# Optimization experiments

Hardware: AMD Instinct MI355X
Metric: run time of the kernel (lower is better)

## Reference

```python
import jax, jax.numpy as jnp
import numpy as np

PAD_ID = 0
B, S, T = 32, 128, 16   # batch, words per sentence, chars per word
VOCAB, E, H = 262, 64, 256


def _lstm_scan(x, w_ih, w_hh, b):
    # x: [T, N, D] -> outputs h: [T, N, H]. PyTorch gate order i, f, g, o.
    N = x.shape[1]
    Hh = w_hh.shape[1]
    init = (jnp.zeros((N, Hh), x.dtype), jnp.zeros((N, Hh), x.dtype))

    def step(carry, xt):
        h, c = carry
        g = xt @ w_ih.T + h @ w_hh.T + b
        i, f, gg, o = jnp.split(g, 4, axis=-1)
        c = jax.nn.sigmoid(f) * c + jax.nn.sigmoid(i) * jnp.tanh(gg)
        h = jax.nn.sigmoid(o) * jnp.tanh(c)
        return (h, c), h

    _, hs = jax.lax.scan(step, init, x)
    return hs


def _bilstm_layer(x, pf, pb):
    # x: [T, N, D]; returns [T, N, 2H] (fwd outputs || time-aligned bwd outputs)
    hf = _lstm_scan(x, *pf)
    hb = _lstm_scan(x[::-1], *pb)[::-1]
    return jnp.concatenate([hf, hb], axis=-1)


def setup_inputs() -> dict:
    key = jax.random.key(0)
    ks = iter(jax.random.split(key, 32))

    def xav(shape):
        fan_in, fan_out = shape[1], shape[0]
        std = float(np.sqrt(2.0 / (fan_in + fan_out)))
        return jax.random.normal(next(ks), shape, dtype=jnp.float32) * std

    char_ids = jax.random.randint(next(ks), (B, S, T), 0, VOCAB, dtype=jnp.int64)
    char_emb = xav((VOCAB, E)).at[PAD_ID].set(0.0)

    inp = {"char_ids": char_ids, "char_emb": char_emb}
    # layer 0 input dim E, layer 1 input dim 2H
    for layer, din in ((0, E), (1, 2 * H)):
        for d in ("f", "b"):
            inp[f"w_ih_l{layer}{d}"] = xav((4 * H, din))
            inp[f"w_hh_l{layer}{d}"] = xav((4 * H, H))
            inp[f"b_l{layer}{d}"] = jnp.ones((4 * H,), dtype=jnp.float32) * 2.0  # b_ih + b_hh, both init to 1
    inp["w_out"] = xav((H, 2 * H))
    inp["b_out"] = jnp.ones((H,), dtype=jnp.float32)
    return inp


def reference(char_ids, char_emb,
              w_ih_l0f, w_hh_l0f, b_l0f, w_ih_l0b, w_hh_l0b, b_l0b,
              w_ih_l1f, w_hh_l1f, b_l1f, w_ih_l1b, w_hh_l1b, b_l1b,
              w_out, b_out):
    b, s, t = char_ids.shape
    n = b * s
    # The torch loop runs the biLSTM independently per word; batching all
    # words together is mathematically identical (no cross-word state).
    x = char_emb[char_ids.reshape(n, t)]            # [N, T, E]
    x = jnp.transpose(x, (1, 0, 2))                 # [T, N, E]
    h0 = _bilstm_layer(x, (w_ih_l0f, w_hh_l0f, b_l0f), (w_ih_l0b, w_hh_l0b, b_l0b))
    h1 = _bilstm_layer(h0, (w_ih_l1f, w_hh_l1f, b_l1f), (w_ih_l1b, w_hh_l1b, b_l1b))
    # torch code takes forward output at t=0 and backward output at t=T-1
    merged = jnp.concatenate([h1[0, :, :H], h1[-1, :, H:]], axis=-1)  # [N, 2H]
    out = merged @ w_out.T + b_out                  # [N, H]
    return out.reshape(b, s, H)
```

## Files before the change

kernel.cpp:

```cpp
#include <hip/hip_runtime.h>


typedef short bf16x8 __attribute__((ext_vector_type(8)));
typedef float f32x4 __attribute__((ext_vector_type(4)));
typedef unsigned short u16;

#define MFMA16(a, b, c) __builtin_amdgcn_mfma_f32_16x16x32_bf16((a), (b), (c), 0, 0, 0)

__device__ __forceinline__ float b2f(u16 u) {
    union { unsigned int i; float f; } v; v.i = ((unsigned int)u) << 16; return v.f;
}
__device__ __forceinline__ u16 f2b(float f) {
    union { float f; unsigned int i; } v; v.f = f;
    unsigned int r = v.i + 0x7fffu + ((v.i >> 16) & 1u);
    return (u16)(r >> 16);
}
__device__ __forceinline__ float cl30(float x) { return fminf(30.0f, fmaxf(-30.0f, x)); }
__device__ __forceinline__ float sigm(float x) { return 1.0f / (1.0f + __expf(-x)); }
__device__ __forceinline__ float tanh_(float x) { return 2.0f / (1.0f + __expf(-2.0f * x)) - 1.0f; }

constexpr int T = 16, E = 64, H = 256, VOCAB = 262;
constexpr int M = 32;
constexpr int XP = 68;
constexpr int HP = 260;
constexpr int NW = 4096;

constexpr int N_IDS = NW * T;
constexpr size_t AB = (size_t)N_IDS * 2;
constexpr size_t O_EMB  = 0;        constexpr int N_EMB  = VOCAB * 64;
constexpr size_t O_WI0F = 16768;    constexpr int N_WI0  = 1024 * 64;
constexpr size_t O_WH0F = 82304;    constexpr int N_WH0  = 1024 * 256;
constexpr size_t O_B0F  = 344448;   constexpr int N_B    = 1024;
constexpr size_t O_WI0B = 345472;
constexpr size_t O_WH0B = 411008;
constexpr size_t O_B0B  = 673152;
constexpr size_t O_WI1F = 674176;   constexpr int N_WI1  = 1024 * 512;
constexpr size_t O_B1F  = 1198464;
constexpr size_t O_WI1B = 1199488;
constexpr size_t O_B1B  = 1723776;
constexpr size_t O_WOUT = 1724800;  constexpr int N_WOUT = 256 * 512;
constexpr size_t O_BOUT = 1855872;  constexpr int N_BOUT = 256;
constexpr size_t ARENA_U16 = 1856128;
constexpr size_t WS_NEED = AB * 2 + ARENA_U16 * 2;

template <bool F32>
__device__ __forceinline__ bf16x8 ldB(const void* p, size_t off) {
    if constexpr (F32) {
        const float* f = (const float*)p + off;
        f32x4 a = *(const f32x4*)f;
        f32x4 b = *(const f32x4*)(f + 4);
        bf16x8 r;
        r[0] = (short)f2b(a[0]); r[1] = (short)f2b(a[1]);
        r[2] = (short)f2b(a[2]); r[3] = (short)f2b(a[3]);
        r[4] = (short)f2b(b[0]); r[5] = (short)f2b(b[1]);
        r[6] = (short)f2b(b[2]); r[7] = (short)f2b(b[3]);
        return r;
    } else {
        return *(const bf16x8*)((const u16*)p + off);
    }
}
template <bool F32>
__device__ __forceinline__ float ldS(const void* p, int i) {
    return F32 ? ((const float*)p)[i] : b2f(((const u16*)p)[i]);
}

__device__ __forceinline__ void seg_cvt(const void* src, u16* dst, int n,
                                        bool f32, int gid, int gsz) {
    if (f32) {
        const float* s = (const float*)src;
        for (int i = gid; i < n; i += gsz) dst[i] = f2b(s[i]);
    } else {
        const u16* s = (const u16*)src;
        for (int i = gid; i < n; i += gsz) dst[i] = s[i];
    }
}

template <bool F32>
__device__ __forceinline__ void frag_cvt(const void* src, u16* dst, int N, int K,
                                         int gid, int gsz) {
    const int KT = K >> 5;
    const int CT = (N >= 256) ? (N >> 8) : 1;
    const int groups = (N * K) >> 3;
    for (int i = gid; i < groups; i += gsz) {
        const int r  = (int)(((long long)i << 3) / K);
        const int k0 = (int)(((long long)i << 3) - (long long)r * K);
        const int w16 = (r >> 4) & 15;
        const int ct  = r >> 8;
        const int l15 = r & 15;
        const int kk  = k0 >> 5;
        const int q   = (k0 >> 3) & 3;
        bf16x8 v = ldB<F32>(src, (size_t)i * 8);
        const size_t chunk = ((size_t)w16 * KT + kk) * CT + ct;
        *(bf16x8*)&dst[chunk * 512 + (size_t)(q * 16 + l15) * 8] = v;
    }
}

__global__ void k_cvt(const int* __restrict__ ids_raw,
                      const void* emb,
                      const void* wi0f, const void* wh0f, const void* b0f,
                      const void* wi0b, const void* wh0b, const void* b0b,
                      const void* wi1f, const void* b1f,
                      const void* wi1b, const void* b1b,
                      const void* wout, const void* bout,
                      int* __restrict__ ids_out, u16* __restrict__ arena)
{
    const int gid = blockIdx.x * blockDim.x + threadIdx.x;
    const int gsz = gridDim.x * blockDim.x;
    const bool f32 = (((const unsigned*)bout)[0] == 0x3F800000u);
    unsigned odd = 0;
#pragma unroll
    for (int k = 1; k < 32; k += 2) odd |= (unsigned)ids_raw[k];
    const bool i64 = (odd == 0u);
    for (int i = gid; i < N_IDS; i += gsz) {
        int id = i64 ? ids_raw[2 * i] : ids_raw[i];
        ids_out[i] = (id < 0) ? 0 : (id >= VOCAB ? VOCAB - 1 : id);
    }
    seg_cvt(emb, arena + O_EMB, N_EMB, f32, gid, gsz);
    if (f32) {
        frag_cvt<true>(wi0f, arena + O_WI0F, 1024, 64,  gid, gsz);
        frag_cvt<true>(wh0f, arena + O_WH0F, 1024, 256, gid, gsz);
        frag_cvt<true>(wi0b, arena + O_WI0B, 1024, 64,  gid, gsz);
        frag_cvt<true>(wh0b, arena + O_WH0B, 1024, 256, gid, gsz);
        frag_cvt<true>(wi1f, arena + O_WI1F, 1024, 512, gid, gsz);
        frag_cvt<true>(wi1b, arena + O_WI1B, 1024, 512, gid, gsz);
        frag_cvt<true>(wout, arena + O_WOUT, 256,  512, gid, gsz);
    } else {
        frag_cvt<false>(wi0f, arena + O_WI0F, 1024, 64,  gid, gsz);
        frag_cvt<false>(wh0f, arena + O_WH0F, 1024, 256, gid, gsz);
        frag_cvt<false>(wi0b, arena + O_WI0B, 1024, 64,  gid, gsz);
        frag_cvt<false>(wh0b, arena + O_WH0B, 1024, 256, gid, gsz);
        frag_cvt<false>(wi1f, arena + O_WI1F, 1024, 512, gid, gsz);
        frag_cvt<false>(wi1b, arena + O_WI1B, 1024, 512, gid, gsz);
        frag_cvt<false>(wout, arena + O_WOUT, 256,  512, gid, gsz);
    }
    seg_cvt(b0f,  arena + O_B0F,  N_B,    f32, gid, gsz);
    seg_cvt(b0b,  arena + O_B0B,  N_B,    f32, gid, gsz);
    seg_cvt(b1f,  arena + O_B1F,  N_B,    f32, gid, gsz);
    seg_cvt(b1b,  arena + O_B1B,  N_B,    f32, gid, gsz);
    seg_cvt(bout, arena + O_BOUT, N_BOUT, f32, gid, gsz);
}

constexpr int LXB0 = 0;
constexpr int LXB1 = LXB0 + M * XP;
constexpr int LHB0 = LXB1 + M * XP;
constexpr int LHB1 = LHB0 + M * HP;
constexpr int LOH  = LHB1 + M * HP;
constexpr int LMG  = LHB1;
constexpr int LTOT = LOH  + M * HP;

template <bool F32, bool FRAG>
__device__ __forceinline__
void body2(const int* __restrict__ ids, const int i64, const void* emb,
           const void* wihF, const void* whhF, const void* bF,
           const void* wihB, const void* whhB, const void* bB,
           const void* wih1f, const void* b1f,
           const void* wih1b, const void* b1b,
           const void* wout, const void* bout,
           float* __restrict__ out, u16* lds)
{
    const int tid = threadIdx.x;
    const int lane = tid & 63;
    const int w16 = tid >> 6;
    const int l15 = lane & 15;
    const int q   = lane >> 4;
    const int dir = blockIdx.x & 1;
    const int wg0 = (blockIdx.x >> 1) * M;
    const int col = w16 * 16 + l15;

    const void* wih  = dir ? wihB : wihF;
    const void* whh  = dir ? whhB : whhF;
    const void* bia  = dir ? bB : bF;
    const void* wihO = dir ? wihF : wihB;
    const void* biaO = dir ? bF : bB;
    const void* w1   = dir ? wih1f : wih1b;
    const void* b1   = dir ? b1f : b1b;
    const int   koff = dir ? 0 : 256;

    const u16* wih_w  = (const u16*)wih  + (size_t)w16 * 2 * 4 * 512;
    const u16* whh_w  = (const u16*)whh  + (size_t)w16 * 8 * 4 * 512;
    const u16* wihO_w = (const u16*)wihO + (size_t)w16 * 2 * 4 * 512;
    const u16* w1_w   = (const u16*)w1   + (size_t)w16 * 16 * 4 * 512;
    const u16* wout_w = (const u16*)wout + (size_t)w16 * 16 * 512;

    u16* xb0 = lds + LXB0;
    u16* xb1 = lds + LXB1;
    u16* hb0 = lds + LHB0;
    u16* hb1 = lds + LHB1;
    u16* oh  = lds + LOH;
    u16* mg  = lds + LMG;

    for (int i = tid; i < M * HP; i += 1024) hb0[i] = 0;

    auto fid = [&](int idx) -> int {
        int id = i64 ? ids[2 * idx] : ids[idx];
        return (id < 0) ? 0 : (id >= VOCAB ? VOCAB - 1 : id);
    };
    auto stage_x = [&](int time, u16* dst) {
        if (tid < M * 8) {
            const int word = tid >> 3, seg = tid & 7;
            const int id = fid((wg0 + word) * T + time);
            *(bf16x8*)&dst[word * XP + seg * 8] = ldB<F32>(emb, (size_t)id * E + seg * 8);
        }
    };

    float breg[4];
#pragma unroll
    for (int g = 0; g < 4; ++g) breg[g] = ldS<F32>(bia, g * 256 + col);

    float cst[2][4];
#pragma unroll
    for (int mt = 0; mt < 2; ++mt)
#pragma unroll
        for (int r = 0; r < 4; ++r) cst[mt][r] = 0.0f;

    auto ldBi = [&](int i, int ct) -> bf16x8 {
        if constexpr (FRAG) {
            return (i < 2)
                ? *(const bf16x8*)&wih_w[(size_t)(i * 4 + ct) * 512 + lane * 8]
                : *(const bf16x8*)&whh_w[(size_t)((i - 2) * 4 + ct) * 512 + lane * 8];
        } else {
            const int n = ct * 256 + col;
            return (i < 2) ? ldB<F32>(wih, (size_t)n * E + i * 32 + q * 8)
                           : ldB<F32>(whh, (size_t)n * H + (i - 2) * 32 + q * 8);
        }
    };

    stage_x(dir ? T - 1 : 0, xb0);

    bf16x8 Bp[2][4];
#pragma unroll
    for (int ct = 0; ct < 4; ++ct) Bp[0][ct] = ldBi(0, ct);

    __syncthreads();

    for (int ts = 0; ts < T; ++ts) {
        u16* xbc = (ts & 1) ? xb1 : xb0;
        u16* hbc = (ts & 1) ? hb1 : hb0;
        u16* hbn = (ts & 1) ? hb0 : hb1;
        u16* xbn = (ts & 1) ? xb0 : xb1;

        f32x4 acc[4][2];
#pragma unroll
        for (int ct = 0; ct < 4; ++ct) {
            acc[ct][0] = (f32x4){0.f, 0.f, 0.f, 0.f};
            acc[ct][1] = (f32x4){0.f, 0.f, 0.f, 0.f};
        }
        auto ldAi = [&](int i, int half) -> bf16x8 {
            const u16* base = (i < 2) ? xbc : hbc;
            const int st = (i < 2) ? XP : HP;
            const int kk = ((i < 2) ? i : (i - 2)) * 32;
            return *(const bf16x8*)&base[(half * 16 + l15) * st + kk + q * 8];
        };

#pragma unroll
        for (int i = 0; i < 10; ++i) {
            const int cur = i & 1, nxt = cur ^ 1;
            if (i + 1 < 10) {
#pragma unroll
                for (int ct = 0; ct < 4; ++ct) Bp[nxt][ct] = ldBi(i + 1, ct);
            } else {
#pragma unroll
                for (int ct = 0; ct < 4; ++ct) Bp[nxt][ct] = ldBi(0, ct);
            }
            bf16x8 a0 = ldAi(i, 0);
            bf16x8 a1 = ldAi(i, 1);
#pragma unroll
            for (int ct = 0; ct < 4; ++ct) {
                acc[ct][0] = MFMA16(a0, Bp[cur][ct], acc[ct][0]);
                acc[ct][1] = MFMA16(a1, Bp[cur][ct], acc[ct][1]);
            }
        }

#pragma unroll
        for (int mt = 0; mt < 2; ++mt)
#pragma unroll
            for (int r = 0; r < 4; ++r) {
                float iv = cl30(acc[0][mt][r] + breg[0]);
                float fv = cl30(acc[1][mt][r] + breg[1]);
                float gv = cl30(acc[2][mt][r] + breg[2]);
                float ov = cl30(acc[3][mt][r] + breg[3]);
                float c = sigm(fv) * cst[mt][r] + sigm(iv) * tanh_(gv);
                cst[mt][r] = c;
                float h = sigm(ov) * tanh_(c);
                hbn[(mt * 16 + q * 4 + r) * HP + col] = f2b(h);
            }
        if (ts + 1 < T) stage_x(dir ? T - 2 - ts : ts + 1, xbn);
        __syncthreads();
    }
    u16* hbF = hb0;

    stage_x(dir ? 0 : T - 1, xb0);
    __syncthreads();
    {
        f32x4 ra[3][2];
#pragma unroll
        for (int gi = 0; gi < 3; ++gi) {
            ra[gi][0] = (f32x4){0.f, 0.f, 0.f, 0.f};
            ra[gi][1] = (f32x4){0.f, 0.f, 0.f, 0.f};
        }
#pragma unroll
        for (int ks = 0; ks < 2; ++ks) {
            bf16x8 a0 = *(const bf16x8*)&xb0[l15 * XP + ks * 32 + q * 8];
            bf16x8 a1 = *(const bf16x8*)&xb0[(16 + l15) * XP + ks * 32 + q * 8];
#pragma unroll
            for (int gi = 0; gi < 3; ++gi) {
                const int g = (gi == 0) ? 0 : gi + 1;
                bf16x8 b;
                if constexpr (FRAG) {
                    b = *(const bf16x8*)&wihO_w[(size_t)(ks * 4 + g) * 512 + lane * 8];
                } else {
                    const int n = g * 256 + col;
                    b = ldB<F32>(wihO, (size_t)n * E + ks * 32 + q * 8);
                }
                ra[gi][0] = MFMA16(a0, b, ra[gi][0]);
                ra[gi][1] = MFMA16(a1, b, ra[gi][1]);
            }
        }
        const float bi = ldS<F32>(biaO, 0 * 256 + col);
        const float bg = ldS<F32>(biaO, 2 * 256 + col);
        const float bo = ldS<F32>(biaO, 3 * 256 + col);
#pragma unroll
        for (int mt = 0; mt < 2; ++mt)
#pragma unroll
            for (int r = 0; r < 4; ++r) {
                float iv = cl30(ra[0][mt][r] + bi);
                float gv = cl30(ra[1][mt][r] + bg);
                float ov = cl30(ra[2][mt][r] + bo);
                float c = sigm(iv) * tanh_(gv);
                float h = sigm(ov) * tanh_(c);
                oh[(mt * 16 + q * 4 + r) * HP + col] = f2b(h);
            }
    }
    __syncthreads();

    {
        const u16* Alo = dir ? oh : hbF;
        const u16* Ahi = dir ? hbF : oh;
        auto ldB1 = [&](int ks, int j) -> bf16x8 {
            const int g = (j == 0) ? 0 : j + 1;
            if constexpr (FRAG) {
                return *(const bf16x8*)&w1_w[(size_t)(ks * 4 + g) * 512 + lane * 8];
            } else {
                const int n = g * 256 + col;
                return ldB<F32>(w1, (size_t)n * 512 + ks * 32 + q * 8);
            }
        };
        auto ldA1 = [&](int ks, int half) -> bf16x8 {
            const u16* A = (ks < 8) ? Alo : Ahi;
            const int kk = (ks & 7) * 32;
            return *(const bf16x8*)&A[(half * 16 + l15) * HP + kk + q * 8];
        };

        f32x4 ca[3][2];
#pragma unroll
        for (int j = 0; j < 3; ++j) {
            ca[j][0] = (f32x4){0.f, 0.f, 0.f, 0.f};
            ca[j][1] = (f32x4){0.f, 0.f, 0.f, 0.f};
        }
        bf16x8 Bc[2][3];
#pragma unroll
        for (int j = 0; j < 3; ++j) Bc[0][j] = ldB1(0, j);

#pragma unroll
        for (int ks = 0; ks < 16; ++ks) {
            const int cur = ks & 1, nxt = cur ^ 1;
            if (ks + 1 < 16) {
#pragma unroll
                for (int j = 0; j < 3; ++j) Bc[nxt][j] = ldB1(ks + 1, j);
            }
            bf16x8 a0 = ldA1(ks, 0);
            bf16x8 a1 = ldA1(ks, 1);
#pragma unroll
            for (int j = 0; j < 3; ++j) {
                ca[j][0] = MFMA16(a0, Bc[cur][j], ca[j][0]);
                ca[j][1] = MFMA16(a1, Bc[cur][j], ca[j][1]);
            }
        }
        const float bi = ldS<F32>(b1, 0 * 256 + col);
        const float bg = ldS<F32>(b1, 2 * 256 + col);
        const float bo = ldS<F32>(b1, 3 * 256 + col);
#pragma unroll
        for (int mt = 0; mt < 2; ++mt)
#pragma unroll
            for (int r = 0; r < 4; ++r) {
                float iv = cl30(ca[0][mt][r] + bi);
                float gv = cl30(ca[1][mt][r] + bg);
                float ov = cl30(ca[2][mt][r] + bo);
                float c = sigm(iv) * tanh_(gv);
                float h = sigm(ov) * tanh_(c);
                mg[(mt * 16 + q * 4 + r) * HP + col] = f2b(h);
            }
    }
    __syncthreads();

    {
        auto ldBo = [&](int ks) -> bf16x8 {
            if constexpr (FRAG) {
                return *(const bf16x8*)&wout_w[(size_t)((dir ? 0 : 8) + ks) * 512 + lane * 8];
            } else {
                return ldB<F32>(wout, (size_t)col * 512 + koff + ks * 32 + q * 8);
            }
        };
        f32x4 oa[2];
        oa[0] = (f32x4){0.f, 0.f, 0.f, 0.f};
        oa[1] = (f32x4){0.f, 0.f, 0.f, 0.f};

        bf16x8 Bo[2];
        Bo[0] = ldBo(0);

#pragma unroll
        for (int ks = 0; ks < 8; ++ks) {
            const int cur = ks & 1, nxt = cur ^ 1;
            if (ks + 1 < 8) Bo[nxt] = ldBo(ks + 1);
            bf16x8 a0 = *(const bf16x8*)&mg[l15 * HP + ks * 32 + q * 8];
            bf16x8 a1 = *(const bf16x8*)&mg[(16 + l15) * HP + ks * 32 + q * 8];
            oa[0] = MFMA16(a0, Bo[cur], oa[0]);
            oa[1] = MFMA16(a1, Bo[cur], oa[1]);
        }
        const float bo = dir ? ldS<F32>(bout, col) : 0.0f;
#pragma unroll
        for (int mt = 0; mt < 2; ++mt)
#pragma unroll
            for (int r = 0; r < 4; ++r)
                atomicAdd(&out[(size_t)(wg0 + mt * 16 + q * 4 + r) * 256 + col],
                          oa[mt][r] + bo);
    }
}

__global__ __attribute__((amdgpu_flat_work_group_size(1024, 1024)))
           __attribute__((amdgpu_waves_per_eu(4, 4)))
void k_scan_bf16(const int* __restrict__ ids, const void* emb,
                 const void* wihF, const void* whhF, const void* bF,
                 const void* wihB, const void* whhB, const void* bB,
                 const void* wih1f, const void* b1f,
                 const void* wih1b, const void* b1b,
                 const void* wout, const void* bout, float* __restrict__ out)
{
    __shared__ __align__(16) u16 lds[LTOT];
    body2<false, true>(ids, 0, emb, wihF, whhF, bF, wihB, whhB, bB,
                       wih1f, b1f, wih1b, b1b, wout, bout, out, lds);
}

__global__ __attribute__((amdgpu_flat_work_group_size(1024, 1024)))
           __attribute__((amdgpu_waves_per_eu(4, 4)))
void k_scan_raw(const int* __restrict__ ids, const void* emb,
                const void* wihF, const void* whhF, const void* bF,
                const void* wihB, const void* whhB, const void* bB,
                const void* wih1f, const void* b1f,
                const void* wih1b, const void* b1b,
                const void* wout, const void* bout, float* __restrict__ out)
{
    __shared__ __align__(16) u16 lds[LTOT];
    const bool f32 = (((const unsigned*)bout)[0] == 0x3F800000u);
    unsigned odd = 0;
#pragma unroll
    for (int k = 1; k < 32; k += 2) odd |= (unsigned)ids[k];
    const int i64 = (odd == 0u) ? 1 : 0;
    if (f32)
        body2<true, false>(ids, i64, emb, wihF, whhF, bF, wihB, whhB, bB,
                           wih1f, b1f, wih1b, b1b, wout, bout, out, lds);
    else
        body2<false, false>(ids, i64, emb, wihF, whhF, bF, wihB, whhB, bB,
                            wih1f, b1f, wih1b, b1b, wout, bout, out, lds);
}

extern "C" void kernel_launch(void* const* d_in, const int* in_sizes, int n_in,
                              void* d_out, int out_size, void* d_ws, size_t ws_size,
                              hipStream_t stream)
{
    const int* ids = (const int*)d_in[0];
    const void* emb  = d_in[1];
    const void* wi0f = d_in[2];
    const void* wh0f = d_in[3];
    const void* b0f  = d_in[4];
    const void* wi0b = d_in[5];
    const void* wh0b = d_in[6];
    const void* b0b  = d_in[7];
    const void* wi1f = d_in[8];
    const void* b1f  = d_in[10];
    const void* wi1b = d_in[11];
    const void* b1b  = d_in[13];
    const void* wout = d_in[14];
    const void* bout = d_in[15];
    float* out = (float*)d_out;

    hipMemsetAsync(d_out, 0, (size_t)out_size * sizeof(float), stream);

    if (ws_size >= WS_NEED) {
        int* ids_n = (int*)d_ws;
        u16* arena = (u16*)d_ws + AB;
        hipLaunchKernelGGL(k_cvt, dim3(1024), dim3(256), 0, stream,
                           ids, emb, wi0f, wh0f, b0f, wi0b, wh0b, b0b,
                           wi1f, b1f, wi1b, b1b, wout, bout, ids_n, arena);
        hipLaunchKernelGGL(k_scan_bf16, dim3(256), dim3(1024), 0, stream,
                           ids_n, arena + O_EMB,
                           arena + O_WI0F, arena + O_WH0F, arena + O_B0F,
                           arena + O_WI0B, arena + O_WH0B, arena + O_B0B,
                           arena + O_WI1F, arena + O_B1F,
                           arena + O_WI1B, arena + O_B1B,
                           arena + O_WOUT, arena + O_BOUT, out);
    } else {
        hipLaunchKernelGGL(k_scan_raw, dim3(256), dim3(1024), 0, stream,
                           ids, emb, wi0f, wh0f, b0f, wi0b, wh0b, b0b,
                           wi1f, b1f, wi1b, b1b, wout, bout, out);
    }
}
```

Baseline: 352.8 us.

## Prefetch LDS A-fragments and next-step embeddings, use lighter LDS-only barriers

```diff
diff --git a/kernel.cpp b/kernel.cpp
--- a/kernel.cpp
+++ b/kernel.cpp
@@ -6,6 +6,12 @@
 typedef unsigned short u16;
 
 #define MFMA16(a, b, c) __builtin_amdgcn_mfma_f32_16x16x32_bf16((a), (b), (c), 0, 0, 0)
+
+__device__ __forceinline__ void bar_lgkm() {
+    asm volatile("s_waitcnt lgkmcnt(0)" ::: "memory");
+    __builtin_amdgcn_sched_barrier(0);
+    __builtin_amdgcn_s_barrier();
+}
 
 __device__ __forceinline__ float b2f(u16 u) {
     union { unsigned int i; float f; } v; v.i = ((unsigned int)u) << 16; return v.f;
@@ -231,14 +237,22 @@
 #pragma unroll
     for (int ct = 0; ct < 4; ++ct) Bp[0][ct] = ldBi(0, ct);
 
-    __syncthreads();
-
+    bar_lgkm();
+
+    bf16x8 sx;
     for (int ts = 0; ts < T; ++ts) {
         u16* xbc = (ts & 1) ? xb1 : xb0;
         u16* hbc = (ts & 1) ? hb1 : hb0;
         u16* hbn = (ts & 1) ? hb0 : hb1;
         u16* xbn = (ts & 1) ? xb0 : xb1;
 
+        const bool st = (ts + 1 < T) && (tid < M * 8);
+        if (st) {
+            const int word = tid >> 3, seg = tid & 7;
+            const int id = fid((wg0 + word) * T + (dir ? T - 2 - ts : ts + 1));
+            sx = ldB<F32>(emb, (size_t)id * E + seg * 8);
+        }
+
         f32x4 acc[4][2];
 #pragma unroll
         for (int ct = 0; ct < 4; ++ct) {
@@ -247,10 +261,12 @@
         }
         auto ldAi = [&](int i, int half) -> bf16x8 {
             const u16* base = (i < 2) ? xbc : hbc;
-            const int st = (i < 2) ? XP : HP;
+            const int st_ = (i < 2) ? XP : HP;
             const int kk = ((i < 2) ? i : (i - 2)) * 32;
-            return *(const bf16x8*)&base[(half * 16 + l15) * st + kk + q * 8];
+            return *(const bf16x8*)&base[(half * 16 + l15) * st_ + kk + q * 8];
         };
+
+        bf16x8 a0 = ldAi(0, 0), a1 = ldAi(0, 1);
 
 #pragma unroll
         for (int i = 0; i < 10; ++i) {
@@ -262,13 +278,14 @@
 #pragma unroll
                 for (int ct = 0; ct < 4; ++ct) Bp[nxt][ct] = ldBi(0, ct);
             }
-            bf16x8 a0 = ldAi(i, 0);
-            bf16x8 a1 = ldAi(i, 1);
+            bf16x8 na0, na1;
+            if (i + 1 < 10) { na0 = ldAi(i + 1, 0); na1 = ldAi(i + 1, 1); }
 #pragma unroll
             for (int ct = 0; ct < 4; ++ct) {
                 acc[ct][0] = MFMA16(a0, Bp[cur][ct], acc[ct][0]);
                 acc[ct][1] = MFMA16(a1, Bp[cur][ct], acc[ct][1]);
             }
+            a0 = na0; a1 = na1;
         }
 
 #pragma unroll
@@ -284,13 +301,16 @@
                 float h = sigm(ov) * tanh_(c);
                 hbn[(mt * 16 + q * 4 + r) * HP + col] = f2b(h);
             }
-        if (ts + 1 < T) stage_x(dir ? T - 2 - ts : ts + 1, xbn);
-        __syncthreads();
+        if (st) {
+            const int word = tid >> 3, seg = tid & 7;
+            *(bf16x8*)&xbn[word * XP + seg * 8] = sx;
+        }
+        bar_lgkm();
     }
     u16* hbF = hb0;
 
     stage_x(dir ? 0 : T - 1, xb0);
-    __syncthreads();
+    bar_lgkm();
     {
         f32x4 ra[3][2];
 #pragma unroll
@@ -331,7 +351,7 @@
                 oh[(mt * 16 + q * 4 + r) * HP + col] = f2b(h);
             }
     }
-    __syncthreads();
+    bar_lgkm();
 
     {
         const u16* Alo = dir ? oh : hbF;
@@ -360,6 +380,7 @@
         bf16x8 Bc[2][3];
 #pragma unroll
         for (int j = 0; j < 3; ++j) Bc[0][j] = ldB1(0, j);
+        bf16x8 a0 = ldA1(0, 0), a1 = ldA1(0, 1);
 
 #pragma unroll
         for (int ks = 0; ks < 16; ++ks) {
@@ -368,13 +389,14 @@
 #pragma unroll
                 for (int j = 0; j < 3; ++j) Bc[nxt][j] = ldB1(ks + 1, j);
             }
-            bf16x8 a0 = ldA1(ks, 0);
-            bf16x8 a1 = ldA1(ks, 1);
+            bf16x8 na0, na1;
+            if (ks + 1 < 16) { na0 = ldA1(ks + 1, 0); na1 = ldA1(ks + 1, 1); }
 #pragma unroll
             for (int j = 0; j < 3; ++j) {
                 ca[j][0] = MFMA16(a0, Bc[cur][j], ca[j][0]);
                 ca[j][1] = MFMA16(a1, Bc[cur][j], ca[j][1]);
             }
+            a0 = na0; a1 = na1;
         }
         const float bi = ldS<F32>(b1, 0 * 256 + col);
         const float bg = ldS<F32>(b1, 2 * 256 + col);
@@ -391,7 +413,7 @@
                 mg[(mt * 16 + q * 4 + r) * HP + col] = f2b(h);
             }
     }
-    __syncthreads();
+    bar_lgkm();
 
     {
         auto ldBo = [&](int ks) -> bf16x8 {
@@ -407,15 +429,21 @@
 
         bf16x8 Bo[2];
         Bo[0] = ldBo(0);
+        bf16x8 a0 = *(const bf16x8*)&mg[l15 * HP + q * 8];
+        bf16x8 a1 = *(const bf16x8*)&mg[(16 + l15) * HP + q * 8];
 
 #pragma unroll
         for (int ks = 0; ks < 8; ++ks) {
             const int cur = ks & 1, nxt = cur ^ 1;
             if (ks + 1 < 8) Bo[nxt] = ldBo(ks + 1);
-            bf16x8 a0 = *(const bf16x8*)&mg[l15 * HP + ks * 32 + q * 8];
-            bf16x8 a1 = *(const bf16x8*)&mg[(16 + l15) * HP + ks * 32 + q * 8];
+            bf16x8 na0, na1;
+            if (ks + 1 < 8) {
+                na0 = *(const bf16x8*)&mg[l15 * HP + (ks + 1) * 32 + q * 8];
+                na1 = *(const bf16x8*)&mg[(16 + l15) * HP + (ks + 1) * 32 + q * 8];
+            }
             oa[0] = MFMA16(a0, Bo[cur], oa[0]);
             oa[1] = MFMA16(a1, Bo[cur], oa[1]);
+            a0 = na0; a1 = na1;
         }
         const float bo = dir ? ldS<F32>(bout, col) : 0.0f;
 #pragma unroll
```

After: 417.0 us. +18.2%, slower.
